# Kernel optimization log

Hardware: AMD Instinct MI355X
Metric: run time of the kernel (lower is better)

The kernel has to match this reference:

```python
import jax, jax.numpy as jnp
import numpy as np

D = 1024   # cfg.hid (downscaled from 8192)
M = 20000  # cfg.mem_c // 2 (downscaled)
B, LQ = 4, 8
PLAST_S = 0.05
IMPORTANCE = 1.0


def mha_shared_kv(q, kv_k, kv_v, Wi, bi, Wo, bo, nheads):
    """torch nn.MultiheadAttention (batch_first) with batch-shared K/V.
    q: [B,Lq,D]; kv_k/kv_v: [Lk,D] shared across batch (avoids the .repeat()
    materialization in the original torch code while computing identical math)."""
    dh = D // nheads
    Wq, Wk, Wv = jnp.split(Wi, 3, axis=0)
    bq, bk, bv = jnp.split(bi, 3)
    qp = (jnp.einsum('bqd,ed->bqe', q, Wq) + bq) * (dh ** -0.5)
    kp = kv_k @ Wk.T + bk              # [Lk,D]
    vp = kv_v @ Wv.T + bv              # [Lk,D]
    qh = qp.reshape(q.shape[0], q.shape[1], nheads, dh)      # [B,Lq,h,dh]
    kh = kp.reshape(kp.shape[0], nheads, dh)                 # [Lk,h,dh]
    vh = vp.reshape(vp.shape[0], nheads, dh)                 # [Lk,h,dh]
    scores = jnp.einsum('bqhd,khd->bhqk', qh, kh)            # [B,h,Lq,Lk]
    attn = jax.nn.softmax(scores, axis=-1)
    ctx = jnp.einsum('bhqk,khd->bqhd', attn, vh)
    ctx = ctx.reshape(q.shape[0], q.shape[1], D)
    return ctx @ Wo.T + bo


def setup_inputs() -> dict:
    key = jax.random.key(0)
    ks = jax.random.split(key, 16)
    s = 0.02
    return {
        'q':    jax.random.normal(ks[0], (B, LQ, D), jnp.float32),
        'data': jax.random.normal(ks[1], (B, D), jnp.float32),
        'ek':   jax.random.normal(ks[2], (M, D), jnp.float32),
        'ev':   jax.random.normal(ks[3], (M, D), jnp.float32),
        'sk':   jax.random.normal(ks[4], (M, D), jnp.float32),
        'sv':   jax.random.normal(ks[5], (M, D), jnp.float32),
        'wm':   jax.random.normal(ks[6], (10, D), jnp.float32),
        'Wi_e': jax.random.normal(ks[7], (3 * D, D), jnp.float32) * s,
        'bi_e': jnp.zeros((3 * D,), jnp.float32),
        'Wo_e': jax.random.normal(ks[8], (D, D), jnp.float32) * s,
        'bo_e': jnp.zeros((D,), jnp.float32),
        'Wi_s': jax.random.normal(ks[9], (3 * D, D), jnp.float32) * s,
        'bi_s': jnp.zeros((3 * D,), jnp.float32),
        'Wo_s': jax.random.normal(ks[10], (D, D), jnp.float32) * s,
        'bo_s': jnp.zeros((D,), jnp.float32),
        'Wi_w': jax.random.normal(ks[11], (3 * D, D), jnp.float32) * s,
        'bi_w': jnp.zeros((3 * D,), jnp.float32),
        'Wo_w': jax.random.normal(ks[12], (D, D), jnp.float32) * s,
        'bo_w': jnp.zeros((D,), jnp.float32),
        'Wrp':  jax.random.normal(ks[13], (D, 3 * D), jnp.float32) * s,
        'brp':  jnp.zeros((D,), jnp.float32),
        'eu':   jnp.zeros((M,), jnp.float32),
    }


def reference(q, data, ek, ev, sk, sv, wm,
              Wi_e, bi_e, Wo_e, bo_e,
              Wi_s, bi_s, Wo_s, bo_s,
              Wi_w, bi_w, Wo_w, bo_w,
              Wrp, brp, eu):
    # ---- NeuroMemory.read ----
    e_r = mha_shared_kv(q, ek, ev, Wi_e, bi_e, Wo_e, bo_e, 16)
    s_r = mha_shared_kv(q, sk, sv, Wi_s, bi_s, Wo_s, bo_s, 16)
    w_r = mha_shared_kv(q, wm, wm, Wi_w, bi_w, Wo_w, bo_w, 8)
    read_out = jnp.concatenate([e_r, s_r, w_r], axis=-1) @ Wrp.T + brp  # [B,Lq,D]

    # ---- NeuroMemory.write (episodic, Hebbian plasticity update) ----
    scores = data @ ek.T                       # [B,M]
    probs = jax.nn.softmax(scores, axis=-1)    # [B,M]
    upd = probs * (PLAST_S * IMPORTANCE)       # [B,M]
    u = upd.mean(axis=0)[:, None]              # [M,1] (batch-mean update strength)
    d = data.mean(axis=0)[None, :]             # [1,D]
    new_ek = ek * (1.0 - u) + d * u            # [M,D]
    new_ev = ev * (1.0 - u) + d * u            # [M,D]
    new_eu = eu * 0.99 + jax.lax.stop_gradient(probs.sum(axis=0))  # [M]
    return (read_out, new_ek, new_ev, new_eu)
```

## Files before the change

kernel.cpp:

```cpp
#include <hip/hip_runtime.h>
#include <hip/hip_fp16.h>
#include <hip/hip_bf16.h>
#include <cstdint>
#include <cstddef>

#define D_HID 1024
#define MEM_M 20000
#define NBATCH 4
#define BL 32
#define NROWS 512
#define SROWS_E 516
#define SROWS_S 512
#define BK 32
#define LDT 40
#define PV_NC 16

typedef __attribute__((ext_vector_type(8))) short short8;
typedef __attribute__((ext_vector_type(4))) float f32x4;
typedef __attribute__((ext_vector_type(4))) unsigned short us4;

__device__ inline ushort f2bf(float f) {
    __hip_bfloat16 b = __float2bfloat16(f);
    return *reinterpret_cast<ushort*>(&b);
}
__device__ inline float h2f(ushort u) {
    __half h; *reinterpret_cast<ushort*>(&h) = u; return __half2float(h);
}

struct SkDesc  { const float* A; const float* B; int K; int M; };
struct SkDescs { SkDesc d[5]; };
struct RdDesc  { const float* bias; float* dst; int M; int ldc; float alpha; };
struct RdDescs { RdDesc d[5]; };

__global__ __launch_bounds__(256)
void k_skinny(SkDescs ds, float* __restrict__ part)
{
    const int g = blockIdx.z;
    const int kc = blockIdx.y, nkc = gridDim.y;
    const int n0 = blockIdx.x * 64;
    const SkDesc dd = ds.d[g];
    const int K = dd.K, M = dd.M;
    const int k0 = kc * 128;

    __shared__ float As[32][132];
    __shared__ float Bs[64][129];
    const int tid = threadIdx.x;
    {
        const int r = tid >> 3, cbl = (tid & 7) * 16;
        if (r < M) {
            const float* src = dd.A + (size_t)r * K + k0 + cbl;
            #pragma unroll
            for (int i = 0; i < 4; ++i) {
                const float4 v = *(const float4*)(src + i * 4);
                As[r][cbl + i * 4 + 0] = v.x; As[r][cbl + i * 4 + 1] = v.y;
                As[r][cbl + i * 4 + 2] = v.z; As[r][cbl + i * 4 + 3] = v.w;
            }
        } else {
            #pragma unroll
            for (int i = 0; i < 16; ++i) As[r][cbl + i] = 0.f;
        }
    }
    {
        const int r = tid >> 2, cbl = (tid & 3) * 32;
        const float* src = dd.B + (size_t)(n0 + r) * K + k0 + cbl;
        #pragma unroll
        for (int i = 0; i < 8; ++i) {
            const float4 v = *(const float4*)(src + i * 4);
            Bs[r][cbl + i * 4 + 0] = v.x; Bs[r][cbl + i * 4 + 1] = v.y;
            Bs[r][cbl + i * 4 + 2] = v.z; Bs[r][cbl + i * 4 + 3] = v.w;
        }
    }
    __syncthreads();
    const int n = tid & 63, mg = tid >> 6;
    float acc[8];
    #pragma unroll
    for (int i = 0; i < 8; ++i) acc[i] = 0.f;
    #pragma unroll 4
    for (int k = 0; k < 128; k += 4) {
        const float b0 = Bs[n][k + 0], b1 = Bs[n][k + 1];
        const float b2 = Bs[n][k + 2], b3 = Bs[n][k + 3];
        #pragma unroll
        for (int i = 0; i < 8; ++i) {
            const float4 a = *(const float4*)&As[mg * 8 + i][k];
            acc[i] = fmaf(a.x, b0, fmaf(a.y, b1, fmaf(a.z, b2, fmaf(a.w, b3, acc[i]))));
        }
    }
    #pragma unroll
    for (int i = 0; i < 8; ++i)
        part[((size_t)(g * nkc + kc) * 32 + mg * 8 + i) * 1024 + n0 + n] = acc[i];
}

__global__ __launch_bounds__(256)
void k_skred(RdDescs ds, const float* __restrict__ part, int nkc)
{
    const int g = blockIdx.y;
    const int m = blockIdx.x;
    const RdDesc dd = ds.d[g];
    if (m >= dd.M) return;
    const int c = threadIdx.x * 4;
    float4 s = make_float4(0.f, 0.f, 0.f, 0.f);
    for (int kc = 0; kc < nkc; ++kc) {
        const float4 v = *(const float4*)&part[((size_t)(g * nkc + kc) * 32 + m) * 1024 + c];
        s.x += v.x; s.y += v.y; s.z += v.z; s.w += v.w;
    }
    const float4 b = *(const float4*)(dd.bias + c);
    float4 o;
    o.x = (s.x + b.x) * dd.alpha; o.y = (s.y + b.y) * dd.alpha;
    o.z = (s.z + b.z) * dd.alpha; o.w = (s.w + b.w) * dd.alpha;
    *(float4*)(dd.dst + (size_t)m * dd.ldc + c) = o;
}

__global__ __launch_bounds__(256)
void mfma_scores(const float* __restrict__ A_e, const float* __restrict__ ek,
                 const float* __restrict__ A_s, const float* __restrict__ sk,
                 __half* __restrict__ S_e, __half* __restrict__ S_s,
                 const float* __restrict__ c0_e, const float* __restrict__ c0_s)
{
    __shared__ ushort As[128][LDT];
    __shared__ ushort Bs[128][LDT];
    const int tid = threadIdx.x;
    const int i = blockIdx.x + 9 * blockIdx.y;
    const int xcd = i & 7, idx = i >> 3;
    const int wg = (xcd < 5 ? xcd * 177 : 885 + (xcd - 5) * 176) + idx;
    const int mi = wg % 9, nb = wg / 9;
    const int bank = (mi >= 5);
    const int m0 = (bank ? (mi - 5) : mi) * 128;
    const int n0 = nb * 128;
    const float* __restrict__ A = bank ? A_s : A_e;
    const float* __restrict__ B = bank ? sk : ek;
    __half* __restrict__ S = bank ? S_s : S_e;
    const float* __restrict__ c0 = bank ? c0_s : c0_e;
    const int Mreal = bank ? SROWS_S : SROWS_E;

    const int wid = tid >> 6, lane = tid & 63;
    const int wr = (wid >> 1) * 64, wc = (wid & 1) * 64;
    const int l15 = lane & 15, l4 = lane >> 4;

    f32x4 acc[4][4];
    const f32x4 fz = {0.f, 0.f, 0.f, 0.f};
    #pragma unroll
    for (int ii = 0; ii < 4; ++ii)
        #pragma unroll
        for (int j = 0; j < 4; ++j) acc[ii][j] = fz;

    for (int kt = 0; kt < 1024; kt += BK) {
        #pragma unroll
        for (int ii = 0; ii < 4; ++ii) {
            const int idx2 = tid + ii * 256;
            const int row = idx2 >> 3, cc = (idx2 & 7) * 4;
            float4 va = *(const float4*)(A + (size_t)(m0 + row) * 1024 + kt + cc);
            us4 wa; wa.x = f2bf(va.x); wa.y = f2bf(va.y); wa.z = f2bf(va.z); wa.w = f2bf(va.w);
            *(us4*)&As[row][cc] = wa;
            int gb = n0 + row; if (gb > MEM_M - 1) gb = MEM_M - 1;
            float4 vb = *(const float4*)(B + (size_t)gb * 1024 + kt + cc);
            us4 wb; wb.x = f2bf(vb.x); wb.y = f2bf(vb.y); wb.z = f2bf(vb.z); wb.w = f2bf(vb.w);
            *(us4*)&Bs[row][cc] = wb;
        }
        __syncthreads();
        short8 a[4], b[4];
        #pragma unroll
        for (int f = 0; f < 4; ++f) {
            a[f] = *(const short8*)&As[wr + f * 16 + l15][l4 * 8];
            b[f] = *(const short8*)&Bs[wc + f * 16 + l15][l4 * 8];
        }
        #pragma unroll
        for (int ii = 0; ii < 4; ++ii)
            #pragma unroll
            for (int j = 0; j < 4; ++j)
                acc[ii][j] = __builtin_amdgcn_mfma_f32_16x16x32_bf16(a[ii], b[j], acc[ii][j], 0, 0, 0);
        __syncthreads();
    }
    #pragma unroll
    for (int ii = 0; ii < 4; ++ii) {
        #pragma unroll
        for (int r = 0; r < 4; ++r) {
            const int row = m0 + wr + ii * 16 + l4 * 4 + r;
            if (row >= Mreal) continue;
            const float cr = c0[row];
            #pragma unroll
            for (int j = 0; j < 4; ++j) {
                const int col = n0 + wc + j * 16 + l15;
                if (col < MEM_M)
                    S[(size_t)row * MEM_M + col] = __float2half(acc[ii][j][r] + cr);
            }
        }
    }
}

__global__ __launch_bounds__(256)
void mfma_pv(const __half* __restrict__ S_e, const __half* __restrict__ S_s,
             const float* __restrict__ ev, const float* __restrict__ sv,
             const float* __restrict__ mrow,
             float* __restrict__ part)
{
    __shared__ ushort As[128][LDT];
    __shared__ ushort Bs[128][LDT];
    const int tid = threadIdx.x;
    const int z = blockIdx.z;
    const int bank = z >> 4, c = z & 15;
    const __half* __restrict__ P = bank ? S_s : S_e;
    const float* __restrict__ V = bank ? sv : ev;
    const int m0 = blockIdx.y * 128, n0 = blockIdx.x * 128;
    const int ks0 = (c * 625) / PV_NC, ks1 = ((c + 1) * 625) / PV_NC;
    const int wid = tid >> 6, lane = tid & 63;
    const int wr = (wid >> 1) * 64, wc = (wid & 1) * 64;
    const int l15 = lane & 15, l4 = lane >> 4;
    const int kb = (tid & 7) * 4, nb = (tid >> 3) * 4;

    const int r0 = tid >> 2;
    const int mbase = (bank ? (SROWS_E + m0) : m0);
    const float mr0 = mrow[mbase + r0];
    const float mr1 = mrow[mbase + r0 + 64];

    f32x4 acc[4][4];
    const f32x4 fz = {0.f, 0.f, 0.f, 0.f};
    #pragma unroll
    for (int i = 0; i < 4; ++i)
        #pragma unroll
        for (int j = 0; j < 4; ++j) acc[i][j] = fz;

    for (int ks = ks0; ks < ks1; ++ks) {
        const int kt = ks * 32;
        #pragma unroll
        for (int i = 0; i < 2; ++i) {
            const int idx = tid + i * 256;
            const int row = idx >> 2, c8 = (idx & 3) * 8;
            const float mr = i ? mr1 : mr0;
            alignas(16) ushort t[8];
            *(short8*)t = *(const short8*)((const ushort*)P + (size_t)(m0 + row) * MEM_M + kt + c8);
            alignas(16) ushort o[8];
            #pragma unroll
            for (int j = 0; j < 8; ++j) o[j] = f2bf(__expf(h2f(t[j]) - mr));
            *(short8*)&As[row][c8] = *(const short8*)o;
        }
        {
            float4 v0 = *(const float4*)(V + (size_t)(kt + kb + 0) * 1024 + n0 + nb);
            float4 v1 = *(const float4*)(V + (size_t)(kt + kb + 1) * 1024 + n0 + nb);
            float4 v2 = *(const float4*)(V + (size_t)(kt + kb + 2) * 1024 + n0 + nb);
            float4 v3 = *(const float4*)(V + (size_t)(kt + kb + 3) * 1024 + n0 + nb);
            us4 w;
            w.x = f2bf(v0.x); w.y = f2bf(v1.x); w.z = f2bf(v2.x); w.w = f2bf(v3.x);
            *(us4*)&Bs[nb + 0][kb] = w;
            w.x = f2bf(v0.y); w.y = f2bf(v1.y); w.z = f2bf(v2.y); w.w = f2bf(v3.y);
            *(us4*)&Bs[nb + 1][kb] = w;
            w.x = f2bf(v0.z); w.y = f2bf(v1.z); w.z = f2bf(v2.z); w.w = f2bf(v3.z);
            *(us4*)&Bs[nb + 2][kb] = w;
            w.x = f2bf(v0.w); w.y = f2bf(v1.w); w.z = f2bf(v2.w); w.w = f2bf(v3.w);
            *(us4*)&Bs[nb + 3][kb] = w;
        }
        __syncthreads();
        short8 a[4], b[4];
        #pragma unroll
        for (int f = 0; f < 4; ++f) {
            a[f] = *(const short8*)&As[wr + f * 16 + l15][l4 * 8];
            b[f] = *(const short8*)&Bs[wc + f * 16 + l15][l4 * 8];
        }
        #pragma unroll
        for (int i = 0; i < 4; ++i)
            #pragma unroll
            for (int j = 0; j < 4; ++j)
                acc[i][j] = __builtin_amdgcn_mfma_f32_16x16x32_bf16(a[i], b[j], acc[i][j], 0, 0, 0);
        __syncthreads();
    }
    float* __restrict__ po = part + (size_t)z * NROWS * 1024;
    #pragma unroll
    for (int i = 0; i < 4; ++i)
        #pragma unroll
        for (int r = 0; r < 4; ++r) {
            const int row = m0 + wr + i * 16 + l4 * 4 + r;
            #pragma unroll
            for (int j = 0; j < 4; ++j) {
                const int col = n0 + wc + j * 16 + l15;
                po[(size_t)row * 1024 + col] = acc[i][j][r];
            }
        }
}

__global__ __launch_bounds__(256)
void k_T(const float* __restrict__ qp,
         const float* __restrict__ Wi_e, const float* __restrict__ bi_e,
         const float* __restrict__ Wi_s, const float* __restrict__ bi_s,
         float* __restrict__ A_e, float* __restrict__ c0_e,
         float* __restrict__ A_s, float* __restrict__ c0_s)
{
    const int bq = blockIdx.x;
    const int bank = bq >> 6;
    const int h = (bq >> 2) & 15;
    const int q4 = bq & 3;
    const float* qpB = qp + (size_t)bank * BL * D_HID;
    const float* Wk = (bank ? Wi_s : Wi_e) + (size_t)D_HID * D_HID;
    const float* bk = (bank ? bi_s : bi_e) + D_HID;
    float* T  = bank ? A_s : A_e;
    float* c0 = bank ? c0_s : c0_e;

    __shared__ float qs[32][64];
    const int tid = threadIdx.x;
    for (int i = tid; i < 32 * 64; i += 256) {
        const int r = i >> 6, j = i & 63;
        qs[r][j] = qpB[(size_t)r * D_HID + h * 64 + j];
    }
    __syncthreads();
    const int e = q4 * 256 + tid;
    float acc[32];
    #pragma unroll
    for (int r = 0; r < 32; ++r) acc[r] = 0.f;
    for (int j = 0; j < 64; ++j) {
        const float w = Wk[(size_t)(h * 64 + j) * D_HID + e];
        #pragma unroll
        for (int r = 0; r < 32; ++r) acc[r] = fmaf(qs[r][j], w, acc[r]);
    }
    #pragma unroll
    for (int r = 0; r < 32; ++r) T[(size_t)(r * 16 + h) * D_HID + e] = acc[r];
    if (q4 == 0 && tid < 32) {
        float s = 0.f;
        for (int j = 0; j < 64; ++j) s += qs[tid][j] * bk[h * 64 + j];
        c0[tid * 16 + h] = s;
    }
}

__global__ __launch_bounds__(256)
void k_softmax(const __half* __restrict__ S_e, const __half* __restrict__ S_s,
               float* __restrict__ mrow, float* __restrict__ lrow)
{
    const int row = blockIdx.x;
    const ushort* p = (row < SROWS_E) ? (const ushort*)(S_e + (size_t)row * MEM_M)
                                      : (const ushort*)(S_s + (size_t)(row - SROWS_E) * MEM_M);
    __shared__ float red_m[256];
    __shared__ float red_l[256];
    const int tid = threadIdx.x;
    float m = -3.0e38f, l = 0.f;
    for (int c = tid; c < MEM_M / 8; c += 256) {
        alignas(16) ushort t[8];
        *(short8*)t = *(const short8*)(p + c * 8);
        float v[8];
        #pragma unroll
        for (int j = 0; j < 8; ++j) v[j] = h2f(t[j]);
        float cm = v[0];
        #pragma unroll
        for (int j = 1; j < 8; ++j) cm = fmaxf(cm, v[j]);
        const float nm = fmaxf(m, cm);
        float s = 0.f;
        #pragma unroll
        for (int j = 0; j < 8; ++j) s += __expf(v[j] - nm);
        l = l * __expf(m - nm) + s;
        m = nm;
    }
    red_m[tid] = m; red_l[tid] = l; __syncthreads();
    for (int s = 128; s > 0; s >>= 1) {
        if (tid < s) {
            const float m2 = fmaxf(red_m[tid], red_m[tid + s]);
            red_l[tid] = red_l[tid] * __expf(red_m[tid] - m2)
                       + red_l[tid + s] * __expf(red_m[tid + s] - m2);
            red_m[tid] = m2;
        }
        __syncthreads();
    }
    if (tid == 0) { mrow[row] = red_m[0]; lrow[row] = red_l[0]; }
}

__global__ __launch_bounds__(256)
void k_uk(const __half* __restrict__ S_e,
          const float* __restrict__ mrow, const float* __restrict__ lrow,
          const float* __restrict__ eu,
          float* __restrict__ u, float* __restrict__ out_eu)
{
    const int k = blockIdx.x * 256 + threadIdx.x;
    if (k >= MEM_M) return;
    float sp = 0.f;
    #pragma unroll
    for (int b = 0; b < NBATCH; ++b) {
        const int row = NROWS + b;
        sp += __expf(__half2float(S_e[(size_t)row * MEM_M + k]) - mrow[row]) / lrow[row];
    }
    u[k] = 0.05f * 0.25f * sp;
    out_eu[k] = eu[k] * 0.99f + sp;
}

__global__ __launch_bounds__(1024)
void k_prep(const float* __restrict__ data, float* __restrict__ A_e,
            float* __restrict__ c0_e, float* __restrict__ dmean)
{
    const int t = threadIdx.x;
    float s = 0.f;
    #pragma unroll
    for (int b = 0; b < NBATCH; ++b) s += data[b * D_HID + t];
    dmean[t] = 0.25f * s;
    #pragma unroll
    for (int b = 0; b < NBATCH; ++b)
        A_e[(size_t)(NROWS + b) * D_HID + t] = data[b * D_HID + t];
    if (t < NBATCH) c0_e[NROWS + t] = 0.f;
}

__global__ __launch_bounds__(256)
void k_zero(float* __restrict__ A_e)
{
    const int row = SROWS_E + blockIdx.x;
    float4* p = (float4*)(A_e + (size_t)row * D_HID);
    p[threadIdx.x] = make_float4(0.f, 0.f, 0.f, 0.f);
}

__global__ __launch_bounds__(256)
void k_pv_reduce(const float* __restrict__ part, const float* __restrict__ lrow,
                 float* __restrict__ R)
{
    const size_t perb4 = (size_t)NROWS * 1024 / 4;
    const size_t i = (size_t)blockIdx.x * 256 + threadIdx.x;
    if (i >= 2 * perb4) return;
    const int bank = i >= perb4;
    const size_t off4 = i - (size_t)bank * perb4;
    const int m = (int)(off4 >> 8);
    const float inv = 1.f / lrow[bank ? (SROWS_E + m) : m];
    const float4* p = (const float4*)part + (size_t)bank * PV_NC * perb4 + off4;
    float4 s = make_float4(0.f, 0.f, 0.f, 0.f);
    #pragma unroll
    for (int c = 0; c < PV_NC; ++c) {
        const float4 v = p[(size_t)c * perb4];
        s.x += v.x; s.y += v.y; s.z += v.z; s.w += v.w;
    }
    s.x *= inv; s.y *= inv; s.z *= inv; s.w *= inv;
    ((float4*)R)[i] = s;
}

__global__ __launch_bounds__(256)
void k_ctx(const float* __restrict__ R,
           const float* __restrict__ Wi_e, const float* __restrict__ bi_e,
           const float* __restrict__ Wi_s, const float* __restrict__ bi_s,
           float* __restrict__ ctx)
{
    const int bank = blockIdx.x >> 4;
    const int h = blockIdx.x & 15;
    const float* Rb = R + (size_t)bank * NROWS * D_HID;
    const float* Wv = (bank ? Wi_s : Wi_e) + (size_t)2 * D_HID * D_HID;
    const float* bv = (bank ? bi_s : bi_e) + 2 * D_HID;
    float* cb = ctx + (size_t)bank * BL * D_HID;
    __shared__ float Rs[32][129];
    __shared__ float Ws[64][129];
    const int tid = threadIdx.x;
    const int j = tid & 63;
    const int g = tid >> 6;
    float acc[8];
    #pragma unroll
    for (int i = 0; i < 8; ++i) acc[i] = 0.f;
    for (int ec = 0; ec < D_HID; ec += 128) {
        for (int i = tid; i < 32 * 128; i += 256) {
            const int r = i >> 7, e = i & 127;
            Rs[r][e] = Rb[(size_t)(r * 16 + h) * D_HID + ec + e];
        }
        for (int i = tid; i < 64 * 128; i += 256) {
            const int r = i >> 7, e = i & 127;
            Ws[r][e] = Wv[(size_t)(h * 64 + r) * D_HID + ec + e];
        }
        __syncthreads();
        for (int e = 0; e < 128; ++e) {
            const float w = Ws[j][e];
            #pragma unroll
            for (int i = 0; i < 8; ++i)
                acc[i] = fmaf(Rs[g + 4 * i][e], w, acc[i]);
        }
        __syncthreads();
    }
    #pragma unroll
    for (int i = 0; i < 8; ++i) {
        const int bl = g + 4 * i;
        cb[(size_t)bl * D_HID + h * 64 + j] = acc[i] + bv[h * 64 + j];
    }
}

__global__ __launch_bounds__(256)
void k_wattn(const float* __restrict__ qp, const float* __restrict__ kpw,
             const float* __restrict__ vpw, float* __restrict__ ctx)
{
    const int bl = blockIdx.x;
    __shared__ float q[D_HID];
    __shared__ float kp[10][D_HID];
    __shared__ float p[8][10];
    const int tid = threadIdx.x;
    const float* qrow = qp + (size_t)(2 * BL + bl) * D_HID;
    for (int i = tid; i < D_HID; i += 256) q[i] = qrow[i];
    for (int i = tid; i < 10 * D_HID; i += 256) kp[i >> 10][i & 1023] = kpw[i];
    __syncthreads();
    if (tid < 80) {
        const int h = tid / 10, k = tid % 10;
        float s = 0.f;
        for (int jj = 0; jj < 128; ++jj) s += q[h * 128 + jj] * kp[k][h * 128 + jj];
        p[h][k] = s;
    }
    __syncthreads();
    if (tid < 8) {
        float m = -3.0e38f;
        for (int k = 0; k < 10; ++k) m = fmaxf(m, p[tid][k]);
        float e[10]; float l = 0.f;
        for (int k = 0; k < 10; ++k) { e[k] = __expf(p[tid][k] - m); l += e[k]; }
        const float inv = 1.f / l;
        for (int k = 0; k < 10; ++k) p[tid][k] = e[k] * inv;
    }
    __syncthreads();
    float* cw = ctx + (size_t)(2 * BL + bl) * D_HID;
    for (int f = tid; f < D_HID; f += 256) {
        const int h = f >> 7;
        float s = 0.f;
        #pragma unroll
        for (int k = 0; k < 10; ++k) s += p[h][k] * vpw[(size_t)k * D_HID + f];
        cw[f] = s;
    }
}

__global__ __launch_bounds__(256)
void k_update(const float* __restrict__ ek, const float* __restrict__ ev,
              const float* __restrict__ u, const float* __restrict__ dmean,
              float* __restrict__ out_ek, float* __restrict__ out_ev)
{
    const size_t n4 = (size_t)MEM_M * D_HID / 4;
    for (size_t i = (size_t)blockIdx.x * 256 + threadIdx.x; i < n4;
         i += (size_t)gridDim.x * 256) {
        const int k = (int)(i >> 8);
        const int c = (int)(i & 255);
        const float uk = u[k];
        const float om = 1.f - uk;
        const float4 dd = ((const float4*)dmean)[c];
        const float4 a = ((const float4*)ek)[i];
        const float4 b = ((const float4*)ev)[i];
        float4 oa, ob;
        oa.x = a.x * om + dd.x * uk; oa.y = a.y * om + dd.y * uk;
        oa.z = a.z * om + dd.z * uk; oa.w = a.w * om + dd.w * uk;
        ob.x = b.x * om + dd.x * uk; ob.y = b.y * om + dd.y * uk;
        ob.z = b.z * om + dd.z * uk; ob.w = b.w * om + dd.w * uk;
        ((float4*)out_ek)[i] = oa;
        ((float4*)out_ev)[i] = ob;
    }
}

extern "C" void kernel_launch(void* const* d_in, const int* in_sizes, int n_in,
                              void* d_out, int out_size, void* d_ws, size_t ws_size,
                              hipStream_t stream)
{
    (void)in_sizes; (void)n_in; (void)out_size; (void)ws_size;
    const float* q    = (const float*)d_in[0];
    const float* data = (const float*)d_in[1];
    const float* ek   = (const float*)d_in[2];
    const float* ev   = (const float*)d_in[3];
    const float* sk   = (const float*)d_in[4];
    const float* sv   = (const float*)d_in[5];
    const float* wm   = (const float*)d_in[6];
    const float* Wi_e = (const float*)d_in[7];
    const float* bi_e = (const float*)d_in[8];
    const float* Wo_e = (const float*)d_in[9];
    const float* bo_e = (const float*)d_in[10];
    const float* Wi_s = (const float*)d_in[11];
    const float* bi_s = (const float*)d_in[12];
    const float* Wo_s = (const float*)d_in[13];
    const float* bo_s = (const float*)d_in[14];
    const float* Wi_w = (const float*)d_in[15];
    const float* bi_w = (const float*)d_in[16];
    const float* Wo_w = (const float*)d_in[17];
    const float* bo_w = (const float*)d_in[18];
    const float* Wrp  = (const float*)d_in[19];
    const float* brp  = (const float*)d_in[20];
    const float* eu   = (const float*)d_in[21];

    float* out = (float*)d_out;
    float* out_read = out;
    float* out_ek = out + 32768;
    float* out_ev = out_ek + 20480000;
    float* out_eu = out_ev + 20480000;

    float* ws    = (float*)d_ws;
    float* qp    = ws;
    float* A_e   = qp + 98304;
    float* A_s   = A_e + 655360;
    float* c0_e  = A_s + 524288;
    float* c0_s  = c0_e + 640;
    float* dmean = c0_s + 512;
    float* u     = dmean + 1024;
    float* mrow  = u + 20480;
    float* lrow  = mrow + 1032;
    float* kpw   = lrow + 1032;
    float* vpw   = kpw + 10240;
    float* ctx   = vpw + 10240;
    float* cat   = ctx + 98304;
    float* skpart = cat + 98304;
    float* Rbuf  = skpart;

    float* part = out_ek;
    __half* S_e = (__half*)out_ev;
    __half* S_s = S_e + (size_t)SROWS_E * MEM_M;

    const dim3 b256(256);
    const float sc16 = 0.125f;
    const float sc8  = 0.08838834764831845f;

    SkDescs s1;
    s1.d[0] = {q,  Wi_e,            1024, 32};
    s1.d[1] = {q,  Wi_s,            1024, 32};
    s1.d[2] = {q,  Wi_w,            1024, 32};
    s1.d[3] = {wm, Wi_w + 1048576,  1024, 10};
    s1.d[4] = {wm, Wi_w + 2097152,  1024, 10};
    k_skinny<<<dim3(16, 8, 5), b256, 0, stream>>>(s1, skpart);
    RdDescs r1;
    r1.d[0] = {bi_e,        qp,         32, 1024, sc16};
    r1.d[1] = {bi_s,        qp + 32768, 32, 1024, sc16};
    r1.d[2] = {bi_w,        qp + 65536, 32, 1024, sc8};
    r1.d[3] = {bi_w + 1024, kpw,        10, 1024, 1.f};
    r1.d[4] = {bi_w + 2048, vpw,        10, 1024, 1.f};
    k_skred<<<dim3(32, 5), b256, 0, stream>>>(r1, skpart, 8);

    k_prep<<<1, 1024, 0, stream>>>(data, A_e, c0_e, dmean);
    k_zero<<<124, b256, 0, stream>>>(A_e);
    k_T<<<128, b256, 0, stream>>>(qp, Wi_e, bi_e, Wi_s, bi_s, A_e, c0_e, A_s, c0_s);

    mfma_scores<<<dim3(9, 157), b256, 0, stream>>>(A_e, ek, A_s, sk, S_e, S_s, c0_e, c0_s);

    k_softmax<<<SROWS_E + SROWS_S, b256, 0, stream>>>(S_e, S_s, mrow, lrow);
    k_uk<<<79, b256, 0, stream>>>(S_e, mrow, lrow, eu, u, out_eu);

    mfma_pv<<<dim3(8, 4, 2 * PV_NC), b256, 0, stream>>>(S_e, S_s, ev, sv, mrow, part);
    k_pv_reduce<<<1024, b256, 0, stream>>>(part, lrow, Rbuf);

    k_ctx<<<32, b256, 0, stream>>>(Rbuf, Wi_e, bi_e, Wi_s, bi_s, ctx);
    k_wattn<<<32, b256, 0, stream>>>(qp, kpw, vpw, ctx);

    SkDescs s2;
    s2.d[0] = {ctx,         Wo_e, 1024, 32};
    s2.d[1] = {ctx + 32768, Wo_s, 1024, 32};
    s2.d[2] = {ctx + 65536, Wo_w, 1024, 32};
    s2.d[3] = {ctx,         Wo_e, 1024, 32};
    s2.d[4] = {ctx,         Wo_e, 1024, 32};
    k_skinny<<<dim3(16, 8, 3), b256, 0, stream>>>(s2, skpart);
    RdDescs r2;
    r2.d[0] = {bo_e, cat,        32, 3072, 1.f};
    r2.d[1] = {bo_s, cat + 1024, 32, 3072, 1.f};
    r2.d[2] = {bo_w, cat + 2048, 32, 3072, 1.f};
    r2.d[3] = r2.d[0];
    r2.d[4] = r2.d[0];
    k_skred<<<dim3(32, 3), b256, 0, stream>>>(r2, skpart, 8);

    SkDescs s3;
    s3.d[0] = {cat, Wrp, 3072, 32};
    s3.d[1] = s3.d[0]; s3.d[2] = s3.d[0]; s3.d[3] = s3.d[0]; s3.d[4] = s3.d[0];
    k_skinny<<<dim3(16, 24, 1), b256, 0, stream>>>(s3, skpart);
    RdDescs r3;
    r3.d[0] = {brp, out_read, 32, 1024, 1.f};
    r3.d[1] = r3.d[0]; r3.d[2] = r3.d[0]; r3.d[3] = r3.d[0]; r3.d[4] = r3.d[0];
    k_skred<<<dim3(32, 1), b256, 0, stream>>>(r3, skpart, 24);

    k_update<<<2048, b256, 0, stream>>>(ek, ev, u, dmean, out_ek, out_ev);
}
```

Before: 547.7 us.

## Double-buffer MFMA GEMMs, pre-convert operands to bf16, fuse tail kernels

```diff
diff --git a/kernel.cpp b/kernel.cpp
--- a/kernel.cpp
+++ b/kernel.cpp
@@ -111,22 +111,22 @@
 }
 
 __global__ __launch_bounds__(256)
-void mfma_scores(const float* __restrict__ A_e, const float* __restrict__ ek,
-                 const float* __restrict__ A_s, const float* __restrict__ sk,
+void mfma_scores(const ushort* __restrict__ A_e, const float* __restrict__ ek,
+                 const ushort* __restrict__ A_s, const float* __restrict__ sk,
                  __half* __restrict__ S_e, __half* __restrict__ S_s,
                  const float* __restrict__ c0_e, const float* __restrict__ c0_s)
 {
-    __shared__ ushort As[128][LDT];
-    __shared__ ushort Bs[128][LDT];
+    __shared__ ushort As[2][128][LDT];
+    __shared__ ushort Bs[2][128][LDT];
     const int tid = threadIdx.x;
     const int i = blockIdx.x + 9 * blockIdx.y;
     const int xcd = i & 7, idx = i >> 3;
     const int wg = (xcd < 5 ? xcd * 177 : 885 + (xcd - 5) * 176) + idx;
-    const int mi = wg % 9, nb = wg / 9;
+    const int mi = wg % 9, nbk = wg / 9;
     const int bank = (mi >= 5);
     const int m0 = (bank ? (mi - 5) : mi) * 128;
-    const int n0 = nb * 128;
-    const float* __restrict__ A = bank ? A_s : A_e;
+    const int n0 = nbk * 128;
+    const ushort* __restrict__ A = bank ? A_s : A_e;
     const float* __restrict__ B = bank ? sk : ek;
     __half* __restrict__ S = bank ? S_s : S_e;
     const float* __restrict__ c0 = bank ? c0_s : c0_e;
@@ -136,6 +136,12 @@
     const int wr = (wid >> 1) * 64, wc = (wid & 1) * 64;
     const int l15 = lane & 15, l4 = lane >> 4;
 
+    const int srow = tid >> 1;
+    const int ac = (tid & 1) * 16;
+    int gbrow = n0 + srow; if (gbrow > MEM_M - 1) gbrow = MEM_M - 1;
+    const ushort* Ap = A + (size_t)(m0 + srow) * 1024 + ac;
+    const float*  Bp = B + (size_t)gbrow * 1024 + ac;
+
     f32x4 acc[4][4];
     const f32x4 fz = {0.f, 0.f, 0.f, 0.f};
     #pragma unroll
@@ -143,32 +149,59 @@
         #pragma unroll
         for (int j = 0; j < 4; ++j) acc[ii][j] = fz;
 
+    short8 ra0 = *(const short8*)(Ap + 0);
+    short8 ra1 = *(const short8*)(Ap + 8);
+    float4 rb0 = *(const float4*)(Bp + 0);
+    float4 rb1 = *(const float4*)(Bp + 4);
+    float4 rb2 = *(const float4*)(Bp + 8);
+    float4 rb3 = *(const float4*)(Bp + 12);
+    *(short8*)&As[0][srow][ac]     = ra0;
+    *(short8*)&As[0][srow][ac + 8] = ra1;
+    {
+        alignas(16) ushort tb[16];
+        tb[0]=f2bf(rb0.x); tb[1]=f2bf(rb0.y); tb[2]=f2bf(rb0.z); tb[3]=f2bf(rb0.w);
+        tb[4]=f2bf(rb1.x); tb[5]=f2bf(rb1.y); tb[6]=f2bf(rb1.z); tb[7]=f2bf(rb1.w);
+        tb[8]=f2bf(rb2.x); tb[9]=f2bf(rb2.y); tb[10]=f2bf(rb2.z); tb[11]=f2bf(rb2.w);
+        tb[12]=f2bf(rb3.x); tb[13]=f2bf(rb3.y); tb[14]=f2bf(rb3.z); tb[15]=f2bf(rb3.w);
+        *(short8*)&Bs[0][srow][ac]     = *(short8*)&tb[0];
+        *(short8*)&Bs[0][srow][ac + 8] = *(short8*)&tb[8];
+    }
+    __syncthreads();
+    int cur = 0;
     for (int kt = 0; kt < 1024; kt += BK) {
-        #pragma unroll
-        for (int ii = 0; ii < 4; ++ii) {
-            const int idx2 = tid + ii * 256;
-            const int row = idx2 >> 3, cc = (idx2 & 7) * 4;
-            float4 va = *(const float4*)(A + (size_t)(m0 + row) * 1024 + kt + cc);
-            us4 wa; wa.x = f2bf(va.x); wa.y = f2bf(va.y); wa.z = f2bf(va.z); wa.w = f2bf(va.w);
-            *(us4*)&As[row][cc] = wa;
-            int gb = n0 + row; if (gb > MEM_M - 1) gb = MEM_M - 1;
-            float4 vb = *(const float4*)(B + (size_t)gb * 1024 + kt + cc);
-            us4 wb; wb.x = f2bf(vb.x); wb.y = f2bf(vb.y); wb.z = f2bf(vb.z); wb.w = f2bf(vb.w);
-            *(us4*)&Bs[row][cc] = wb;
-        }
-        __syncthreads();
+        const bool more = (kt + BK) < 1024;
+        if (more) {
+            ra0 = *(const short8*)(Ap + kt + BK);
+            ra1 = *(const short8*)(Ap + kt + BK + 8);
+            rb0 = *(const float4*)(Bp + kt + BK);
+            rb1 = *(const float4*)(Bp + kt + BK + 4);
+            rb2 = *(const float4*)(Bp + kt + BK + 8);
+            rb3 = *(const float4*)(Bp + kt + BK + 12);
+        }
         short8 a[4], b[4];
         #pragma unroll
         for (int f = 0; f < 4; ++f) {
-            a[f] = *(const short8*)&As[wr + f * 16 + l15][l4 * 8];
-            b[f] = *(const short8*)&Bs[wc + f * 16 + l15][l4 * 8];
+            a[f] = *(const short8*)&As[cur][wr + f * 16 + l15][l4 * 8];
+            b[f] = *(const short8*)&Bs[cur][wc + f * 16 + l15][l4 * 8];
         }
         #pragma unroll
         for (int ii = 0; ii < 4; ++ii)
             #pragma unroll
             for (int j = 0; j < 4; ++j)
                 acc[ii][j] = __builtin_amdgcn_mfma_f32_16x16x32_bf16(a[ii], b[j], acc[ii][j], 0, 0, 0);
+        if (more) {
+            *(short8*)&As[cur ^ 1][srow][ac]     = ra0;
+            *(short8*)&As[cur ^ 1][srow][ac + 8] = ra1;
+            alignas(16) ushort tb[16];
+            tb[0]=f2bf(rb0.x); tb[1]=f2bf(rb0.y); tb[2]=f2bf(rb0.z); tb[3]=f2bf(rb0.w);
+            tb[4]=f2bf(rb1.x); tb[5]=f2bf(rb1.y); tb[6]=f2bf(rb1.z); tb[7]=f2bf(rb1.w);
+            tb[8]=f2bf(rb2.x); tb[9]=f2bf(rb2.y); tb[10]=f2bf(rb2.z); tb[11]=f2bf(rb2.w);
+            tb[12]=f2bf(rb3.x); tb[13]=f2bf(rb3.y); tb[14]=f2bf(rb3.z); tb[15]=f2bf(rb3.w);
+            *(short8*)&Bs[cur ^ 1][srow][ac]     = *(short8*)&tb[0];
+            *(short8*)&Bs[cur ^ 1][srow][ac + 8] = *(short8*)&tb[8];
+        }
         __syncthreads();
+        cur ^= 1;
     }
     #pragma unroll
     for (int ii = 0; ii < 4; ++ii) {
@@ -188,29 +221,25 @@
 }
 
 __global__ __launch_bounds__(256)
-void mfma_pv(const __half* __restrict__ S_e, const __half* __restrict__ S_s,
+void mfma_pv(const ushort* __restrict__ P_e, const ushort* __restrict__ P_s,
              const float* __restrict__ ev, const float* __restrict__ sv,
-             const float* __restrict__ mrow,
              float* __restrict__ part)
 {
-    __shared__ ushort As[128][LDT];
-    __shared__ ushort Bs[128][LDT];
+    __shared__ ushort As[2][128][LDT];
+    __shared__ ushort Bs[2][128][LDT];
     const int tid = threadIdx.x;
     const int z = blockIdx.z;
     const int bank = z >> 4, c = z & 15;
-    const __half* __restrict__ P = bank ? S_s : S_e;
+    const ushort* __restrict__ P = bank ? P_s : P_e;
     const float* __restrict__ V = bank ? sv : ev;
     const int m0 = blockIdx.y * 128, n0 = blockIdx.x * 128;
     const int ks0 = (c * 625) / PV_NC, ks1 = ((c + 1) * 625) / PV_NC;
     const int wid = tid >> 6, lane = tid & 63;
     const int wr = (wid >> 1) * 64, wc = (wid & 1) * 64;
     const int l15 = lane & 15, l4 = lane >> 4;
-    const int kb = (tid & 7) * 4, nb = (tid >> 3) * 4;
-
-    const int r0 = tid >> 2;
-    const int mbase = (bank ? (SROWS_E + m0) : m0);
-    const float mr0 = mrow[mbase + r0];
-    const float mr1 = mrow[mbase + r0 + 64];
+    const int kb = (tid & 7) * 4, nb2 = (tid >> 3) * 4;
+    const int srow = tid >> 1, ac = (tid & 1) * 16;
+    const ushort* Pp = P + (size_t)(m0 + srow) * MEM_M + ac;
 
     f32x4 acc[4][4];
     const f32x4 fz = {0.f, 0.f, 0.f, 0.f};
@@ -219,48 +248,65 @@
         #pragma unroll
         for (int j = 0; j < 4; ++j) acc[i][j] = fz;
 
+    const int kt0 = ks0 * 32;
+    short8 ra0 = *(const short8*)(Pp + kt0);
+    short8 ra1 = *(const short8*)(Pp + kt0 + 8);
+    float4 rb0 = *(const float4*)(V + (size_t)(kt0 + kb + 0) * 1024 + n0 + nb2);
+    float4 rb1 = *(const float4*)(V + (size_t)(kt0 + kb + 1) * 1024 + n0 + nb2);
+    float4 rb2 = *(const float4*)(V + (size_t)(kt0 + kb + 2) * 1024 + n0 + nb2);
+    float4 rb3 = *(const float4*)(V + (size_t)(kt0 + kb + 3) * 1024 + n0 + nb2);
+    *(short8*)&As[0][srow][ac]     = ra0;
+    *(short8*)&As[0][srow][ac + 8] = ra1;
+    {
+        us4 w;
+        w.x = f2bf(rb0.x); w.y = f2bf(rb1.x); w.z = f2bf(rb2.x); w.w = f2bf(rb3.x);
+        *(us4*)&Bs[0][nb2 + 0][kb] = w;
+        w.x = f2bf(rb0.y); w.y = f2bf(rb1.y); w.z = f2bf(rb2.y); w.w = f2bf(rb3.y);
+        *(us4*)&Bs[0][nb2 + 1][kb] = w;
+        w.x = f2bf(rb0.z); w.y = f2bf(rb1.z); w.z = f2bf(rb2.z); w.w = f2bf(rb3.z);
+        *(us4*)&Bs[0][nb2 + 2][kb] = w;
+        w.x = f2bf(rb0.w); w.y = f2bf(rb1.w); w.z = f2bf(rb2.w); w.w = f2bf(rb3.w);
+        *(us4*)&Bs[0][nb2 + 3][kb] = w;
+    }
+    __syncthreads();
+    int cur = 0;
     for (int ks = ks0; ks < ks1; ++ks) {
-        const int kt = ks * 32;
-        #pragma unroll
-        for (int i = 0; i < 2; ++i) {
-            const int idx = tid + i * 256;
-            const int row = idx >> 2, c8 = (idx & 3) * 8;
-            const float mr = i ? mr1 : mr0;
-            alignas(16) ushort t[8];
-            *(short8*)t = *(const short8*)((const ushort*)P + (size_t)(m0 + row) * MEM_M + kt + c8);
-            alignas(16) ushort o[8];
-            #pragma unroll
-            for (int j = 0; j < 8; ++j) o[j] = f2bf(__expf(h2f(t[j]) - mr));
-            *(short8*)&As[row][c8] = *(const short8*)o;
-        }
-        {
-            float4 v0 = *(const float4*)(V + (size_t)(kt + kb + 0) * 1024 + n0 + nb);
-            float4 v1 = *(const float4*)(V + (size_t)(kt + kb + 1) * 1024 + n0 + nb);
-            float4 v2 = *(const float4*)(V + (size_t)(kt + kb + 2) * 1024 + n0 + nb);
-            float4 v3 = *(const float4*)(V + (size_t)(kt + kb + 3) * 1024 + n0 + nb);
-            us4 w;
-            w.x = f2bf(v0.x); w.y = f2bf(v1.x); w.z = f2bf(v2.x); w.w = f2bf(v3.x);
-            *(us4*)&Bs[nb + 0][kb] = w;
-            w.x = f2bf(v0.y); w.y = f2bf(v1.y); w.z = f2bf(v2.y); w.w = f2bf(v3.y);
-            *(us4*)&Bs[nb + 1][kb] = w;
-            w.x = f2bf(v0.z); w.y = f2bf(v1.z); w.z = f2bf(v2.z); w.w = f2bf(v3.z);
-            *(us4*)&Bs[nb + 2][kb] = w;
-            w.x = f2bf(v0.w); w.y = f2bf(v1.w); w.z = f2bf(v2.w); w.w = f2bf(v3.w);
-            *(us4*)&Bs[nb + 3][kb] = w;
-        }
-        __syncthreads();
+        const bool more = (ks + 1) < ks1;
+        if (more) {
+            const int kt = (ks + 1) * 32;
+            ra0 = *(const short8*)(Pp + kt);
+            ra1 = *(const short8*)(Pp + kt + 8);
+            rb0 = *(const float4*)(V + (size_t)(kt + kb + 0) * 1024 + n0 + nb2);
+            rb1 = *(const float4*)(V + (size_t)(kt + kb + 1) * 1024 + n0 + nb2);
+            rb2 = *(const float4*)(V + (size_t)(kt + kb + 2) * 1024 + n0 + nb2);
+            rb3 = *(const float4*)(V + (size_t)(kt + kb + 3) * 1024 + n0 + nb2);
+        }
         short8 a[4], b[4];
         #pragma unroll
         for (int f = 0; f < 4; ++f) {
-            a[f] = *(const short8*)&As[wr + f * 16 + l15][l4 * 8];
-            b[f] = *(const short8*)&Bs[wc + f * 16 + l15][l4 * 8];
+            a[f] = *(const short8*)&As[cur][wr + f * 16 + l15][l4 * 8];
+            b[f] = *(const short8*)&Bs[cur][wc + f * 16 + l15][l4 * 8];
         }
         #pragma unroll
         for (int i = 0; i < 4; ++i)
             #pragma unroll
             for (int j = 0; j < 4; ++j)
                 acc[i][j] = __builtin_amdgcn_mfma_f32_16x16x32_bf16(a[i], b[j], acc[i][j], 0, 0, 0);
+        if (more) {
+            *(short8*)&As[cur ^ 1][srow][ac]     = ra0;
+            *(short8*)&As[cur ^ 1][srow][ac + 8] = ra1;
+            us4 w;
+            w.x = f2bf(rb0.x); w.y = f2bf(rb1.x); w.z = f2bf(rb2.x); w.w = f2bf(rb3.x);
+            *(us4*)&Bs[cur ^ 1][nb2 + 0][kb] = w;
+            w.x = f2bf(rb0.y); w.y = f2bf(rb1.y); w.z = f2bf(rb2.y); w.w = f2bf(rb3.y);
+            *(us4*)&Bs[cur ^ 1][nb2 + 1][kb] = w;
+            w.x = f2bf(rb0.z); w.y = f2bf(rb1.z); w.z = f2bf(rb2.z); w.w = f2bf(rb3.z);
+            *(us4*)&Bs[cur ^ 1][nb2 + 2][kb] = w;
+            w.x = f2bf(rb0.w); w.y = f2bf(rb1.w); w.z = f2bf(rb2.w); w.w = f2bf(rb3.w);
+            *(us4*)&Bs[cur ^ 1][nb2 + 3][kb] = w;
+        }
         __syncthreads();
+        cur ^= 1;
     }
     float* __restrict__ po = part + (size_t)z * NROWS * 1024;
     #pragma unroll
@@ -280,21 +326,41 @@
 void k_T(const float* __restrict__ qp,
          const float* __restrict__ Wi_e, const float* __restrict__ bi_e,
          const float* __restrict__ Wi_s, const float* __restrict__ bi_s,
-         float* __restrict__ A_e, float* __restrict__ c0_e,
-         float* __restrict__ A_s, float* __restrict__ c0_s)
+         ushort* __restrict__ A_e, float* __restrict__ c0_e,
+         ushort* __restrict__ A_s, float* __restrict__ c0_s,
+         const float* __restrict__ data, float* __restrict__ dmean)
 {
     const int bq = blockIdx.x;
+    const int tid = threadIdx.x;
+    if (bq >= 128) {
+        if (bq < 252) {
+            const int row = SROWS_E + (bq - 128);
+            us4 z4; z4.x = 0; z4.y = 0; z4.z = 0; z4.w = 0;
+            *(us4*)(A_e + (size_t)row * 1024 + tid * 4) = z4;
+        } else {
+            for (int t = tid; t < D_HID; t += 256) {
+                float s = 0.f;
+                #pragma unroll
+                for (int b = 0; b < NBATCH; ++b) s += data[b * D_HID + t];
+                dmean[t] = 0.25f * s;
+                #pragma unroll
+                for (int b = 0; b < NBATCH; ++b)
+                    A_e[(size_t)(NROWS + b) * 1024 + t] = f2bf(data[b * D_HID + t]);
+            }
+            if (tid < NBATCH) c0_e[NROWS + tid] = 0.f;
+        }
+        return;
+    }
     const int bank = bq >> 6;
     const int h = (bq >> 2) & 15;
     const int q4 = bq & 3;
     const float* qpB = qp + (size_t)bank * BL * D_HID;
     const float* Wk = (bank ? Wi_s : Wi_e) + (size_t)D_HID * D_HID;
     const float* bk = (bank ? bi_s : bi_e) + D_HID;
-    float* T  = bank ? A_s : A_e;
+    ushort* T  = bank ? A_s : A_e;
     float* c0 = bank ? c0_s : c0_e;
 
     __shared__ float qs[32][64];
-    const int tid = threadIdx.x;
     for (int i = tid; i < 32 * 64; i += 256) {
         const int r = i >> 6, j = i & 63;
         qs[r][j] = qpB[(size_t)r * D_HID + h * 64 + j];
@@ -310,7 +376,7 @@
         for (int r = 0; r < 32; ++r) acc[r] = fmaf(qs[r][j], w, acc[r]);
     }
     #pragma unroll
-    for (int r = 0; r < 32; ++r) T[(size_t)(r * 16 + h) * D_HID + e] = acc[r];
+    for (int r = 0; r < 32; ++r) T[(size_t)(r * 16 + h) * 1024 + e] = f2bf(acc[r]);
     if (q4 == 0 && tid < 32) {
         float s = 0.f;
         for (int j = 0; j < 64; ++j) s += qs[tid][j] * bk[h * 64 + j];
@@ -319,12 +385,13 @@
 }
 
 __global__ __launch_bounds__(256)
-void k_softmax(const __half* __restrict__ S_e, const __half* __restrict__ S_s,
+void k_softmax(__half* __restrict__ S_e, __half* __restrict__ S_s,
                float* __restrict__ mrow, float* __restrict__ lrow)
 {
     const int row = blockIdx.x;
-    const ushort* p = (row < SROWS_E) ? (const ushort*)(S_e + (size_t)row * MEM_M)
-                                      : (const ushort*)(S_s + (size_t)(row - SROWS_E) * MEM_M);
+    ushort* p = (row < SROWS_E) ? (ushort*)(S_e + (size_t)row * MEM_M)
+                                : (ushort*)(S_s + (size_t)(row - SROWS_E) * MEM_M);
+    const bool conv = (row < SROWS_E) ? (row < NROWS) : true;
     __shared__ float red_m[256];
     __shared__ float red_l[256];
     const int tid = threadIdx.x;
@@ -355,7 +422,18 @@
         }
         __syncthreads();
     }
-    if (tid == 0) { mrow[row] = red_m[0]; lrow[row] = red_l[0]; }
+    const float rm = red_m[0];
+    if (conv) {
+        for (int c = tid; c < MEM_M / 8; c += 256) {
+            alignas(16) ushort t[8];
+            *(short8*)t = *(const short8*)(p + c * 8);
+            alignas(16) ushort o[8];
+            #pragma unroll
+            for (int j = 0; j < 8; ++j) o[j] = f2bf(__expf(h2f(t[j]) - rm));
+            *(short8*)(p + c * 8) = *(const short8*)o;
+        }
+    }
+    if (tid == 0) { mrow[row] = rm; lrow[row] = red_l[0]; }
 }
 
 __global__ __launch_bounds__(256)
@@ -376,157 +454,145 @@
     out_eu[k] = eu[k] * 0.99f + sp;
 }
 
-__global__ __launch_bounds__(1024)
-void k_prep(const float* __restrict__ data, float* __restrict__ A_e,
-            float* __restrict__ c0_e, float* __restrict__ dmean)
-{
-    const int t = threadIdx.x;
-    float s = 0.f;
-    #pragma unroll
-    for (int b = 0; b < NBATCH; ++b) s += data[b * D_HID + t];
-    dmean[t] = 0.25f * s;
-    #pragma unroll
-    for (int b = 0; b < NBATCH; ++b)
-        A_e[(size_t)(NROWS + b) * D_HID + t] = data[b * D_HID + t];
-    if (t < NBATCH) c0_e[NROWS + t] = 0.f;
-}
-
-__global__ __launch_bounds__(256)
-void k_zero(float* __restrict__ A_e)
-{
-    const int row = SROWS_E + blockIdx.x;
-    float4* p = (float4*)(A_e + (size_t)row * D_HID);
-    p[threadIdx.x] = make_float4(0.f, 0.f, 0.f, 0.f);
-}
-
-__global__ __launch_bounds__(256)
-void k_pv_reduce(const float* __restrict__ part, const float* __restrict__ lrow,
-                 float* __restrict__ R)
-{
-    const size_t perb4 = (size_t)NROWS * 1024 / 4;
-    const size_t i = (size_t)blockIdx.x * 256 + threadIdx.x;
-    if (i >= 2 * perb4) return;
-    const int bank = i >= perb4;
-    const size_t off4 = i - (size_t)bank * perb4;
-    const int m = (int)(off4 >> 8);
-    const float inv = 1.f / lrow[bank ? (SROWS_E + m) : m];
-    const float4* p = (const float4*)part + (size_t)bank * PV_NC * perb4 + off4;
-    float4 s = make_float4(0.f, 0.f, 0.f, 0.f);
-    #pragma unroll
-    for (int c = 0; c < PV_NC; ++c) {
-        const float4 v = p[(size_t)c * perb4];
-        s.x += v.x; s.y += v.y; s.z += v.z; s.w += v.w;
-    }
-    s.x *= inv; s.y *= inv; s.z *= inv; s.w *= inv;
-    ((float4*)R)[i] = s;
-}
-
-__global__ __launch_bounds__(256)
-void k_ctx(const float* __restrict__ R,
-           const float* __restrict__ Wi_e, const float* __restrict__ bi_e,
-           const float* __restrict__ Wi_s, const float* __restrict__ bi_s,
-           float* __restrict__ ctx)
-{
-    const int bank = blockIdx.x >> 4;
-    const int h = blockIdx.x & 15;
-    const float* Rb = R + (size_t)bank * NROWS * D_HID;
-    const float* Wv = (bank ? Wi_s : Wi_e) + (size_t)2 * D_HID * D_HID;
-    const float* bv = (bank ? bi_s : bi_e) + 2 * D_HID;
-    float* cb = ctx + (size_t)bank * BL * D_HID;
-    __shared__ float Rs[32][129];
-    __shared__ float Ws[64][129];
+__global__ __launch_bounds__(256)
+void k_pvred_upd(const float* __restrict__ part, const float* __restrict__ lrow,
+                 float* __restrict__ R,
+                 const float* __restrict__ ev, const float* __restrict__ u,
+                 const float* __restrict__ dmean, float* __restrict__ out_ev)
+{
     const int tid = threadIdx.x;
-    const int j = tid & 63;
-    const int g = tid >> 6;
-    float acc[8];
-    #pragma unroll
-    for (int i = 0; i < 8; ++i) acc[i] = 0.f;
-    for (int ec = 0; ec < D_HID; ec += 128) {
-        for (int i = tid; i < 32 * 128; i += 256) {
-            const int r = i >> 7, e = i & 127;
-            Rs[r][e] = Rb[(size_t)(r * 16 + h) * D_HID + ec + e];
-        }
-        for (int i = tid; i < 64 * 128; i += 256) {
-            const int r = i >> 7, e = i & 127;
-            Ws[r][e] = Wv[(size_t)(h * 64 + r) * D_HID + ec + e];
-        }
+    if (blockIdx.x < 1024) {
+        const size_t perb4 = (size_t)NROWS * 1024 / 4;
+        const size_t i = (size_t)blockIdx.x * 256 + tid;
+        const int bank = i >= perb4;
+        const size_t off4 = i - (size_t)bank * perb4;
+        const int m = (int)(off4 >> 8);
+        const float inv = 1.f / lrow[bank ? (SROWS_E + m) : m];
+        const float4* p = (const float4*)part + (size_t)bank * PV_NC * perb4 + off4;
+        float4 s = make_float4(0.f, 0.f, 0.f, 0.f);
+        #pragma unroll
+        for (int c = 0; c < PV_NC; ++c) {
+            const float4 v = p[(size_t)c * perb4];
+            s.x += v.x; s.y += v.y; s.z += v.z; s.w += v.w;
+        }
+        s.x *= inv; s.y *= inv; s.z *= inv; s.w *= inv;
+        ((float4*)R)[i] = s;
+    } else {
+        const int bid = blockIdx.x - 1024;
+        const size_t n4 = (size_t)MEM_M * D_HID / 4;
+        for (size_t i = (size_t)bid * 256 + tid; i < n4; i += (size_t)1024 * 256) {
+            const int k = (int)(i >> 8);
+            const int c = (int)(i & 255);
+            const float uk = u[k];
+            const float om = 1.f - uk;
+            const float4 dd = ((const float4*)dmean)[c];
+            const float4 b = ((const float4*)ev)[i];
+            float4 ob;
+            ob.x = b.x * om + dd.x * uk; ob.y = b.y * om + dd.y * uk;
+            ob.z = b.z * om + dd.z * uk; ob.w = b.w * om + dd.w * uk;
+            ((float4*)out_ev)[i] = ob;
+        }
+    }
+}
+
+__global__ __launch_bounds__(256)
+void k_tail(const float* __restrict__ R,
+            const float* __restrict__ Wi_e, const float* __restrict__ bi_e,
+            const float* __restrict__ Wi_s, const float* __restrict__ bi_s,
+            float* __restrict__ ctx,
+            const float* __restrict__ qp, const float* __restrict__ kpw,
+            const float* __restrict__ vpw,
+            const float* __restrict__ ek, const float* __restrict__ u,
+            const float* __restrict__ dmean, float* __restrict__ out_ek)
+{
+    __shared__ float sm[12384];
+    const int tid = threadIdx.x;
+    const int bx = blockIdx.x;
+    if (bx < 32) {
+        const int bank = bx >> 4;
+        const int h = bx & 15;
+        const float* Rb = R + (size_t)bank * NROWS * D_HID;
+        const float* Wv = (bank ? Wi_s : Wi_e) + (size_t)2 * D_HID * D_HID;
+        const float* bv = (bank ? bi_s : bi_e) + 2 * D_HID;
+        float* cb = ctx + (size_t)bank * BL * D_HID;
+        float (*Rs)[129] = (float(*)[129])sm;
+        float (*Ws)[129] = (float(*)[129])(sm + 32 * 129);
+        const int j = tid & 63;
+        const int g = tid >> 6;
+        float acc[8];
+        #pragma unroll
+        for (int i = 0; i < 8; ++i) acc[i] = 0.f;
+        for (int ec = 0; ec < D_HID; ec += 128) {
+            for (int i = tid; i < 32 * 128; i += 256) {
+                const int r = i >> 7, e = i & 127;
+                Rs[r][e] = Rb[(size_t)(r * 16 + h) * D_HID + ec + e];
+            }
+            for (int i = tid; i < 64 * 128; i += 256) {
+                const int r = i >> 7, e = i & 127;
+                Ws[r][e] = Wv[(size_t)(h * 64 + r) * D_HID + ec + e];
+            }
+            __syncthreads();
+            for (int e = 0; e < 128; ++e) {
+                const float w = Ws[j][e];
+                #pragma unroll
+                for (int i = 0; i < 8; ++i)
+                    acc[i] = fmaf(Rs[g + 4 * i][e], w, acc[i]);
+            }
+            __syncthreads();
+        }
+        #pragma unroll
+        for (int i = 0; i < 8; ++i) {
+            const int bl = g + 4 * i;
+            cb[(size_t)bl * D_HID + h * 64 + j] = acc[i] + bv[h * 64 + j];
+        }
+    } else if (bx < 64) {
+        const int bl = bx - 32;
+        float* q = sm;
+        float (*kp)[1024] = (float(*)[1024])(sm + 1024);
+        float (*pp)[10] = (float(*)[10])(sm + 1024 + 10240);
+        const float* qrow = qp + (size_t)(2 * BL + bl) * D_HID;
+        for (int i = tid; i < D_HID; i += 256) q[i] = qrow[i];
+        for (int i = tid; i < 10 * D_HID; i += 256) kp[i >> 10][i & 1023] = kpw[i];
         __syncthreads();
-        for (int e = 0; e < 128; ++e) {
-            const float w = Ws[j][e];
+        if (tid < 80) {
+            const int h = tid / 10, k = tid % 10;
+            float s = 0.f;
+            for (int jj = 0; jj < 128; ++jj) s += q[h * 128 + jj] * kp[k][h * 128 + jj];
+            pp[h][k] = s;
+        }
+        __syncthreads();
+        if (tid < 8) {
+            float m = -3.0e38f;
+            for (int k = 0; k < 10; ++k) m = fmaxf(m, pp[tid][k]);
+            float e[10]; float l = 0.f;
+            for (int k = 0; k < 10; ++k) { e[k] = __expf(pp[tid][k] - m); l += e[k]; }
+            const float inv = 1.f / l;
+            for (int k = 0; k < 10; ++k) pp[tid][k] = e[k] * inv;
+        }
+        __syncthreads();
+        float* cw = ctx + (size_t)(2 * BL + bl) * D_HID;
+        for (int f = tid; f < D_HID; f += 256) {
+            const int h = f >> 7;
+            float s = 0.f;
             #pragma unroll
-            for (int i = 0; i < 8; ++i)
-                acc[i] = fmaf(Rs[g + 4 * i][e], w, acc[i]);
-        }
-        __syncthreads();
-    }
-    #pragma unroll
-    for (int i = 0; i < 8; ++i) {
-        const int bl = g + 4 * i;
-        cb[(size_t)bl * D_HID + h * 64 + j] = acc[i] + bv[h * 64 + j];
-    }
-}
-
-__global__ __launch_bounds__(256)
-void k_wattn(const float* __restrict__ qp, const float* __restrict__ kpw,
-             const float* __restrict__ vpw, float* __restrict__ ctx)
-{
-    const int bl = blockIdx.x;
-    __shared__ float q[D_HID];
-    __shared__ float kp[10][D_HID];
-    __shared__ float p[8][10];
-    const int tid = threadIdx.x;
-    const float* qrow = qp + (size_t)(2 * BL + bl) * D_HID;
-    for (int i = tid; i < D_HID; i += 256) q[i] = qrow[i];
-    for (int i = tid; i < 10 * D_HID; i += 256) kp[i >> 10][i & 1023] = kpw[i];
-    __syncthreads();
-    if (tid < 80) {
-        const int h = tid / 10, k = tid % 10;
-        float s = 0.f;
-        for (int jj = 0; jj < 128; ++jj) s += q[h * 128 + jj] * kp[k][h * 128 + jj];
-        p[h][k] = s;
-    }
-    __syncthreads();
-    if (tid < 8) {
-        float m = -3.0e38f;
-        for (int k = 0; k < 10; ++k) m = fmaxf(m, p[tid][k]);
-        float e[10]; float l = 0.f;
-        for (int k = 0; k < 10; ++k) { e[k] = __expf(p[tid][k] - m); l += e[k]; }
-        const float inv = 1.f / l;
-        for (int k = 0; k < 10; ++k) p[tid][k] = e[k] * inv;
-    }
-    __syncthreads();
-    float* cw = ctx + (size_t)(2 * BL + bl) * D_HID;
-    for (int f = tid; f < D_HID; f += 256) {
-        const int h = f >> 7;
-        float s = 0.f;
-        #pragma unroll
-        for (int k = 0; k < 10; ++k) s += p[h][k] * vpw[(size_t)k * D_HID + f];
-        cw[f] = s;
-    }
-}
-
-__global__ __launch_bounds__(256)
-void k_update(const float* __restrict__ ek, const float* __restrict__ ev,
-              const float* __restrict__ u, const float* __restrict__ dmean,
-              float* __restrict__ out_ek, float* __restrict__ out_ev)
-{
-    const size_t n4 = (size_t)MEM_M * D_HID / 4;
-    for (size_t i = (size_t)blockIdx.x * 256 + threadIdx.x; i < n4;
-         i += (size_t)gridDim.x * 256) {
-        const int k = (int)(i >> 8);
-        const int c = (int)(i & 255);
-        const float uk = u[k];
-        const float om = 1.f - uk;
-        const float4 dd = ((const float4*)dmean)[c];
-        const float4 a = ((const float4*)ek)[i];
-        const float4 b = ((const float4*)ev)[i];
-        float4 oa, ob;
-        oa.x = a.x * om + dd.x * uk; oa.y = a.y * om + dd.y * uk;
-        oa.z = a.z * om + dd.z * uk; oa.w = a.w * om + dd.w * uk;
-        ob.x = b.x * om + dd.x * uk; ob.y = b.y * om + dd.y * uk;
-        ob.z = b.z * om + dd.z * uk; ob.w = b.w * om + dd.w * uk;
-        ((float4*)out_ek)[i] = oa;
-        ((float4*)out_ev)[i] = ob;
+            for (int k = 0; k < 10; ++k) s += pp[h][k] * vpw[(size_t)k * D_HID + f];
+            cw[f] = s;
+        }
+    } else {
+        const int bid = bx - 64;
+        const size_t n4 = (size_t)MEM_M * D_HID / 4;
+        for (size_t i = (size_t)bid * 256 + tid; i < n4; i += (size_t)1024 * 256) {
+            const int k = (int)(i >> 8);
+            const int c = (int)(i & 255);
+            const float uk = u[k];
+            const float om = 1.f - uk;
+            const float4 dd = ((const float4*)dmean)[c];
+            const float4 a = ((const float4*)ek)[i];
+            float4 oa;
+            oa.x = a.x * om + dd.x * uk; oa.y = a.y * om + dd.y * uk;
+            oa.z = a.z * om + dd.z * uk; oa.w = a.w * om + dd.w * uk;
+            ((float4*)out_ek)[i] = oa;
+        }
     }
 }
 
@@ -581,6 +647,9 @@
     float* skpart = cat + 98304;
     float* Rbuf  = skpart;
 
+    ushort* A_e16 = (ushort*)A_e;
+    ushort* A_s16 = (ushort*)A_s;
+
     float* part = out_ek;
     __half* S_e = (__half*)out_ev;
     __half* S_s = S_e + (size_t)SROWS_E * MEM_M;
@@ -604,20 +673,21 @@
     r1.d[4] = {bi_w + 2048, vpw,        10, 1024, 1.f};
     k_skred<<<dim3(32, 5), b256, 0, stream>>>(r1, skpart, 8);
 
-    k_prep<<<1, 1024, 0, stream>>>(data, A_e, c0_e, dmean);
-    k_zero<<<124, b256, 0, stream>>>(A_e);
-    k_T<<<128, b256, 0, stream>>>(qp, Wi_e, bi_e, Wi_s, bi_s, A_e, c0_e, A_s, c0_s);
-
-    mfma_scores<<<dim3(9, 157), b256, 0, stream>>>(A_e, ek, A_s, sk, S_e, S_s, c0_e, c0_s);
+    k_T<<<253, b256, 0, stream>>>(qp, Wi_e, bi_e, Wi_s, bi_s,
+                                  A_e16, c0_e, A_s16, c0_s, data, dmean);
+
+    mfma_scores<<<dim3(9, 157), b256, 0, stream>>>(A_e16, ek, A_s16, sk, S_e, S_s, c0_e, c0_s);
 
     k_softmax<<<SROWS_E + SROWS_S, b256, 0, stream>>>(S_e, S_s, mrow, lrow);
     k_uk<<<79, b256, 0, stream>>>(S_e, mrow, lrow, eu, u, out_eu);
 
-    mfma_pv<<<dim3(8, 4, 2 * PV_NC), b256, 0, stream>>>(S_e, S_s, ev, sv, mrow, part);
-    k_pv_reduce<<<1024, b256, 0, stream>>>(part, lrow, Rbuf);
-
-    k_ctx<<<32, b256, 0, stream>>>(Rbuf, Wi_e, bi_e, Wi_s, bi_s, ctx);
-    k_wattn<<<32, b256, 0, stream>>>(qp, kpw, vpw, ctx);
+    mfma_pv<<<dim3(8, 4, 2 * PV_NC), b256, 0, stream>>>((const ushort*)S_e, (const ushort*)S_s,
+                                                        ev, sv, part);
+
+    k_pvred_upd<<<2048, b256, 0, stream>>>(part, lrow, Rbuf, ev, u, dmean, out_ev);
+
+    k_tail<<<1088, b256, 0, stream>>>(Rbuf, Wi_e, bi_e, Wi_s, bi_s, ctx,
+                                      qp, kpw, vpw, ek, u, dmean, out_ek);
 
     SkDescs s2;
     s2.d[0] = {ctx,         Wo_e, 1024, 32};
@@ -643,5 +713,5 @@
     r3.d[1] = r3.d[0]; r3.d[2] = r3.d[0]; r3.d[3] = r3.d[0]; r3.d[4] = r3.d[0];
     k_skred<<<dim3(32, 1), b256, 0, stream>>>(r3, skpart, 24);
 
-    k_update<<<2048, b256, 0, stream>>>(ek, ev, u, dmean, out_ek, out_ev);
-}
+    k_update_done:;
+}
```

After: 526.1 us. 1.04x faster.
